# Kernel tuning notes

Hardware: AMD Instinct MI355X
Metric: run time of the kernel (lower is better)

Reference implementation:

```python
import jax, jax.numpy as jnp
import numpy as np

NUM_GROUPS = 32
EPS = 1e-5


def group_norm(x, gamma, beta):
    b, c, h, w = x.shape
    xg = x.reshape(b, NUM_GROUPS, c // NUM_GROUPS, h, w)
    mu = xg.mean(axis=(2, 3, 4), keepdims=True)
    var = xg.var(axis=(2, 3, 4), keepdims=True)
    xg = (xg - mu) * jax.lax.rsqrt(var + EPS)
    x = xg.reshape(b, c, h, w)
    return x * gamma[None, :, None, None] + beta[None, :, None, None]


def conv1x1(x, w, b):
    # 1x1 conv == per-pixel matmul over channels
    return jnp.einsum('oc,bchw->bohw', w, x) + b[None, :, None, None]


def setup_inputs() -> dict:
    key = jax.random.key(0)
    ks = jax.random.split(key, 6)
    c = 512
    scale = 0.02  # keep logits in a sane range
    return {
        'x': jax.random.normal(ks[0], (2, c, 64, 64), dtype=jnp.float32),
        'gn_w': jnp.ones((c,), jnp.float32),
        'gn_b': jnp.zeros((c,), jnp.float32),
        'wq': jax.random.normal(ks[1], (c, c), jnp.float32) * scale,
        'bq': jnp.zeros((c,), jnp.float32),
        'wk': jax.random.normal(ks[2], (c, c), jnp.float32) * scale,
        'bk': jnp.zeros((c,), jnp.float32),
        'wv': jax.random.normal(ks[3], (c, c), jnp.float32) * scale,
        'bv': jnp.zeros((c,), jnp.float32),
        'wo': jax.random.normal(ks[4], (c, c), jnp.float32) * scale,
        'bo': jnp.zeros((c,), jnp.float32),
    }


def reference(x, gn_w, gn_b, wq, bq, wk, bk, wv, bv, wo, bo):
    b, c, h, w = x.shape
    n = h * w
    h_ = group_norm(x, gn_w, gn_b)
    q = conv1x1(h_, wq, bq).reshape(b, c, n)  # (b,c,n)
    k = conv1x1(h_, wk, bk).reshape(b, c, n)
    v = conv1x1(h_, wv, bv).reshape(b, c, n)
    # scores: (b, n_q, n_k) = q^T k, scaled by c^-0.5
    scores = jnp.einsum('bcq,bck->bqk', q, k) * (c ** -0.5)
    attn = jax.nn.softmax(scores, axis=-1)
    # h_ = v @ attn^T  -> (b, c, n_q)
    out = jnp.einsum('bck,bqk->bcq', v, attn).reshape(b, c, h, w)
    return x + conv1x1(out, wo, bo)
```

## Files before the change

### kernel.cpp

```cpp
#include <hip/hip_runtime.h>

typedef __bf16 bf16_t;
typedef __bf16 bf16x8 __attribute__((ext_vector_type(8)));
typedef __bf16 bf16x4 __attribute__((ext_vector_type(4)));
typedef float  floatx4 __attribute__((ext_vector_type(4)));
typedef int    intx8  __attribute__((ext_vector_type(8)));

#define B_  2
#define C_  512
#define N_  4096
#define EPS 1e-5f
#define SCALE 0.044194173824159216f

__device__ __forceinline__ void gl2lds16(const void* g, void* l) {
  __builtin_amdgcn_global_load_lds(
      (const __attribute__((address_space(1))) void*)g,
      (__attribute__((address_space(3))) void*)l, 16, 0, 0);
}

__device__ __forceinline__ unsigned char f8(float x) {
  return (unsigned char)(__builtin_amdgcn_cvt_pk_fp8_f32(x, x, 0, false) & 0xff);
}

__device__ __forceinline__ floatx4 mfma128_fp8(intx8 a, intx8 b, floatx4 c) {
  return __builtin_amdgcn_mfma_scale_f32_16x16x128_f8f6f4(
      a, b, c, 0, 0, 0, 127, 0, 127);
}

union Frag32 { uint4 q[2]; intx8 v; };

template <int BM, int BN>
__device__ __forceinline__ void gemm_main(
    const bf16_t* __restrict__ A, const bf16_t* __restrict__ B, int K,
    int m0, int n0, floatx4 (&acc)[BM / 32][BN / 32],
    bf16_t* __restrict__ As, bf16_t* __restrict__ Bs) {
  const int tid = threadIdx.x;
  const int w = tid >> 6, l = tid & 63;
  const int wm = (w >> 1) * (BM / 2), wn = (w & 1) * (BN / 2);
  const int lrow = l & 15, lq = l >> 4;
  const int key = lrow & 7;
  const int slot0 = lq ^ key;
  const int slot1 = (4 + lq) ^ key;

  floatx4 zero = {0.f, 0.f, 0.f, 0.f};
#pragma unroll
  for (int mm = 0; mm < BM / 32; mm++)
#pragma unroll
    for (int nn = 0; nn < BN / 32; nn++) acc[mm][nn] = zero;

  for (int k0 = 0; k0 < K; k0 += 64) {
#pragma unroll
    for (int p = 0; p < BM / 32; p++) {
      int gch = p * 256 + tid;
      int r = gch >> 3;
      int cg = (gch & 7) ^ (r & 7);
      gl2lds16(A + (size_t)(m0 + r) * K + k0 + cg * 8, As + gch * 8);
    }
#pragma unroll
    for (int p = 0; p < BN / 32; p++) {
      int gch = p * 256 + tid;
      int r = gch >> 3;
      int cg = (gch & 7) ^ (r & 7);
      gl2lds16(B + (size_t)(n0 + r) * K + k0 + cg * 8, Bs + gch * 8);
    }
    __syncthreads();

    bf16x8 af[BM / 32][2], bfr[BN / 32][2];
#pragma unroll
    for (int mm = 0; mm < BM / 32; mm++) {
      int row = wm + mm * 16 + lrow;
      af[mm][0] = *(const bf16x8*)(As + row * 64 + slot0 * 8);
      af[mm][1] = *(const bf16x8*)(As + row * 64 + slot1 * 8);
    }
#pragma unroll
    for (int nn = 0; nn < BN / 32; nn++) {
      int row = wn + nn * 16 + lrow;
      bfr[nn][0] = *(const bf16x8*)(Bs + row * 64 + slot0 * 8);
      bfr[nn][1] = *(const bf16x8*)(Bs + row * 64 + slot1 * 8);
    }
#pragma unroll
    for (int h = 0; h < 2; h++)
#pragma unroll
      for (int mm = 0; mm < BM / 32; mm++)
#pragma unroll
        for (int nn = 0; nn < BN / 32; nn++)
          acc[mm][nn] = __builtin_amdgcn_mfma_f32_16x16x32_bf16(
              af[mm][h], bfr[nn][h], acc[mm][nn], 0, 0, 0);
    __syncthreads();
  }
}

__global__ __launch_bounds__(256) void gemm_qkv(
    const bf16_t* __restrict__ Wqkv, const bf16_t* __restrict__ h_t,
    unsigned char* __restrict__ q8, unsigned char* __restrict__ k8,
    unsigned char* __restrict__ v8,
    const float* __restrict__ bq, const float* __restrict__ bk,
    const float* __restrict__ bv) {
  __shared__ __align__(16) char smem[32768];
  floatx4 acc[4][4];
  const int m0 = blockIdx.y * 128, n0 = blockIdx.x * 128;
  gemm_main<128, 128>(Wqkv, h_t, 512, m0, n0, acc,
                      (bf16_t*)smem, (bf16_t*)(smem + 16384));

  const int tid = threadIdx.x, w = tid >> 6, l = tid & 63;
  const int wm = (w >> 1) * 64, wn = (w & 1) * 64;
  const int lrow = l & 15, q4 = (l >> 4) * 4;
  const int mat = m0 >> 9;
  const float* bias = (mat == 0) ? bq : (mat == 1) ? bk : bv;

  if (mat < 2) {
    unsigned char* ot = (mat == 0) ? q8 : k8;
#pragma unroll
    for (int mm = 0; mm < 4; mm++) {
#pragma unroll
      for (int nn = 0; nn < 4; nn++) {
        int n = n0 + wn + nn * 16 + lrow;
        int mloc = m0 - mat * 512 + wm + mm * 16 + q4;
        floatx4 a = acc[mm][nn];
        float v0 = a[0] + bias[mloc + 0];
        float v1 = a[1] + bias[mloc + 1];
        float v2 = a[2] + bias[mloc + 2];
        float v3 = a[3] + bias[mloc + 3];
        unsigned int p = __builtin_amdgcn_cvt_pk_fp8_f32(v0, v1, 0, false);
        p = __builtin_amdgcn_cvt_pk_fp8_f32(v2, v3, p, true);
        *(unsigned int*)(ot + (size_t)n * 512 + mloc) = p;
      }
    }
  } else {
    unsigned char* tile8 = (unsigned char*)smem;
#pragma unroll
    for (int mm = 0; mm < 4; mm++) {
#pragma unroll
      for (int nn = 0; nn < 4; nn++) {
        int colp = wn + nn * 16 + lrow;
        floatx4 a = acc[mm][nn];
#pragma unroll
        for (int r = 0; r < 4; r++) {
          int row = wm + mm * 16 + q4 + r;
          int ch = (colp >> 4) ^ ((row >> 2) & 7);
          tile8[row * 128 + ch * 16 + (colp & 15)] =
              f8(a[r] + bias[m0 - 1024 + row]);
        }
      }
    }
    __syncthreads();
    const int bb = n0 >> 12, nl0 = n0 & 4095;
    const int mloc0 = m0 - 1024;
#pragma unroll
    for (int i = 0; i < 4; i++) {
      int c = i * 256 + tid;
      int row = c >> 3, k = c & 7;
      int ch = k ^ ((row >> 2) & 7);
      uint4 d = *(const uint4*)(tile8 + row * 128 + ch * 16);
      *(uint4*)(v8 + (size_t)bb * (C_ * N_) + (size_t)(mloc0 + row) * N_ +
                nl0 + k * 16) = d;
    }
  }
}

__global__ __launch_bounds__(256) void gemm_scores(
    const unsigned char* __restrict__ q8, const unsigned char* __restrict__ k8,
    unsigned char* __restrict__ S8, size_t sstride, float* __restrict__ L,
    int zbase, int nz) {
  __shared__ __align__(16) unsigned char As[128 * 128];
  __shared__ __align__(16) unsigned char Bs[128 * 128];
  const int id = blockIdx.x;
  const int x = id & 7, s = id >> 3;
  const int mi = s & 3, n = (s >> 2) & 31;
  const int zloc = (nz == 2) ? (s >> 7) : 0;
  const int z = (nz == 2) ? zloc : zbase;
  const int m = x * 4 + mi;
  const int m0 = m * 128, n0 = n * 128;

  const unsigned char* A = k8 + (size_t)z * (N_ * C_);
  const unsigned char* B = q8 + (size_t)z * (N_ * C_);
  unsigned char* Sb = S8 + (size_t)zloc * sstride;
  float* Lb = L + (size_t)zloc * N_;

  const int tid = threadIdx.x;
  const int w = tid >> 6, l = tid & 63;
  const int wm = (w >> 1) * 64, wn = (w & 1) * 64;
  const int lrow = l & 15, lq = l >> 4;
  const int key = lrow & 7;
  const int e0 = (2 * lq) ^ key;

  floatx4 acc[4][4];
  floatx4 zero = {0.f, 0.f, 0.f, 0.f};
#pragma unroll
  for (int mm = 0; mm < 4; mm++)
#pragma unroll
    for (int nn = 0; nn < 4; nn++) acc[mm][nn] = zero;

  for (int k0 = 0; k0 < C_; k0 += 128) {
#pragma unroll
    for (int p = 0; p < 4; p++) {
      int gch = p * 256 + tid;
      int r = gch >> 3;
      int cg = (gch & 7) ^ (r & 7);
      gl2lds16(A + (size_t)(m0 + r) * C_ + k0 + cg * 16, As + gch * 16);
    }
#pragma unroll
    for (int p = 0; p < 4; p++) {
      int gch = p * 256 + tid;
      int r = gch >> 3;
      int cg = (gch & 7) ^ (r & 7);
      gl2lds16(B + (size_t)(n0 + r) * C_ + k0 + cg * 16, Bs + gch * 16);
    }
    __syncthreads();

    intx8 af[4], bfr[4];
#pragma unroll
    for (int mm = 0; mm < 4; mm++) {
      int row = wm + mm * 16 + lrow;
      Frag32 f;
      f.q[0] = *(const uint4*)(As + row * 128 + e0 * 16);
      f.q[1] = *(const uint4*)(As + row * 128 + (e0 ^ 1) * 16);
      af[mm] = f.v;
    }
#pragma unroll
    for (int nn = 0; nn < 4; nn++) {
      int row = wn + nn * 16 + lrow;
      Frag32 f;
      f.q[0] = *(const uint4*)(Bs + row * 128 + e0 * 16);
      f.q[1] = *(const uint4*)(Bs + row * 128 + (e0 ^ 1) * 16);
      bfr[nn] = f.v;
    }
#pragma unroll
    for (int mm = 0; mm < 4; mm++)
#pragma unroll
      for (int nn = 0; nn < 4; nn++)
        acc[mm][nn] = mfma128_fp8(af[mm], bfr[nn], acc[mm][nn]);
    __syncthreads();
  }

  float lsum[4] = {0.f, 0.f, 0.f, 0.f};
#pragma unroll
  for (int mm = 0; mm < 4; mm++) {
#pragma unroll
    for (int nn = 0; nn < 4; nn++) {
      int i  = n0 + wn + nn * 16 + lrow;
      int jb = m0 + wm + mm * 16 + lq * 4;
      floatx4 a = acc[mm][nn];
      float e0v = __expf(a[0] * SCALE);
      float e1v = __expf(a[1] * SCALE);
      float e2v = __expf(a[2] * SCALE);
      float e3v = __expf(a[3] * SCALE);
      lsum[nn] += (e0v + e1v) + (e2v + e3v);
      unsigned int p = __builtin_amdgcn_cvt_pk_fp8_f32(e0v, e1v, 0, false);
      p = __builtin_amdgcn_cvt_pk_fp8_f32(e2v, e3v, p, true);
      *(unsigned int*)(Sb + (size_t)i * N_ + jb) = p;
    }
  }
#pragma unroll
  for (int nn = 0; nn < 4; nn++) {
    float vsum = lsum[nn];
    vsum += __shfl_xor(vsum, 16);
    vsum += __shfl_xor(vsum, 32);
    if (lq == 0)
      atomicAdd(Lb + n0 + wn + nn * 16 + lrow, vsum);
  }
}

__global__ __launch_bounds__(512) void gemm_pv(
    const unsigned char* __restrict__ S8, size_t sstride,
    const unsigned char* __restrict__ v8, const float* __restrict__ L,
    bf16_t* __restrict__ O_t, int zbase, int nz) {
  __shared__ __align__(16) char smem[49152];
  const int id = blockIdx.x;
  int nb, mb, zloc;
  if (nz == 2) { nb = id >> 6; int g = id & 63; mb = g >> 1; zloc = g & 1; }
  else         { nb = id >> 5; mb = id & 31; zloc = 0; }
  const int z = (nz == 2) ? zloc : zbase;

  const unsigned char* A = S8 + (size_t)zloc * sstride;
  const unsigned char* B = v8 + (size_t)z * (C_ * N_);
  const float* Lb = L + (size_t)zloc * N_;
  const int m0 = mb * 128, n0 = nb * 64;

  const int tid = threadIdx.x;
  const int w = tid >> 6, l = tid & 63;
  const int wk = w >> 2;
  const int wl = w & 3;
  const int t2 = tid & 255;
  unsigned char* Ah = (unsigned char*)smem + wk * (128 * 128);
  unsigned char* Bh = (unsigned char*)(smem + 32768) + wk * (64 * 128);

  const int wm = (wl >> 1) * 64, wn = (wl & 1) * 32;
  const int lrow = l & 15, lq = l >> 4;
  const int key = lrow & 7;
  const int e0 = (2 * lq) ^ key;

  floatx4 acc[4][2];
  floatx4 zero = {0.f, 0.f, 0.f, 0.f};
#pragma unroll
  for (int mm = 0; mm < 4; mm++)
#pragma unroll
    for (int nn = 0; nn < 2; nn++) acc[mm][nn] = zero;

  const int kbase = wk * 2048;
  for (int kk = 0; kk < 2048; kk += 128) {
    const int k0 = kbase + kk;
#pragma unroll
    for (int p = 0; p < 4; p++) {
      int gch = p * 256 + t2;
      int r = gch >> 3;
      int cg = (gch & 7) ^ (r & 7);
      gl2lds16(A + (size_t)(m0 + r) * 4096 + k0 + cg * 16, Ah + gch * 16);
    }
#pragma unroll
    for (int p = 0; p < 2; p++) {
      int gch = p * 256 + t2;
      int r = gch >> 3;
      int cg = (gch & 7) ^ (r & 7);
      gl2lds16(B + (size_t)(n0 + r) * 4096 + k0 + cg * 16, Bh + gch * 16);
    }
    __syncthreads();

    intx8 af[4], bfr[2];
#pragma unroll
    for (int mm = 0; mm < 4; mm++) {
      int row = wm + mm * 16 + lrow;
      Frag32 f;
      f.q[0] = *(const uint4*)(Ah + row * 128 + e0 * 16);
      f.q[1] = *(const uint4*)(Ah + row * 128 + (e0 ^ 1) * 16);
      af[mm] = f.v;
    }
#pragma unroll
    for (int nn = 0; nn < 2; nn++) {
      int row = wn + nn * 16 + lrow;
      Frag32 f;
      f.q[0] = *(const uint4*)(Bh + row * 128 + e0 * 16);
      f.q[1] = *(const uint4*)(Bh + row * 128 + (e0 ^ 1) * 16);
      bfr[nn] = f.v;
    }
#pragma unroll
    for (int mm = 0; mm < 4; mm++)
#pragma unroll
      for (int nn = 0; nn < 2; nn++)
        acc[mm][nn] = mfma128_fp8(af[mm], bfr[nn], acc[mm][nn]);
    __syncthreads();
  }

  floatx4* buf = (floatx4*)smem;
  const int lanebase = wl * 64 + l;
  if (wk == 1) {
#pragma unroll
    for (int mm = 0; mm < 4; mm++)
#pragma unroll
      for (int nn = 0; nn < 2; nn++)
        buf[(mm * 2 + nn) * 256 + lanebase] = acc[mm][nn];
  }
  __syncthreads();

  bf16_t* tile = (bf16_t*)(smem + 32768);
  if (wk == 0) {
    const int q4 = lq * 4;
#pragma unroll
    for (int mm = 0; mm < 4; mm++) {
      const int rowb = wm + mm * 16 + q4;
      float rv0 = 1.0f / Lb[m0 + rowb + 0];
      float rv1 = 1.0f / Lb[m0 + rowb + 1];
      float rv2 = 1.0f / Lb[m0 + rowb + 2];
      float rv3 = 1.0f / Lb[m0 + rowb + 3];
#pragma unroll
      for (int nn = 0; nn < 2; nn++) {
        floatx4 a = acc[mm][nn] + buf[(mm * 2 + nn) * 256 + lanebase];
        a[0] *= rv0; a[1] *= rv1; a[2] *= rv2; a[3] *= rv3;
        int colp = wn + nn * 16 + lrow;
#pragma unroll
        for (int r = 0; r < 4; r++) {
          int row = rowb + r;
          int ch = (colp >> 3) ^ ((row >> 2) & 7);
          tile[row * 64 + ch * 8 + (colp & 7)] = (bf16_t)a[r];
        }
      }
    }
  }
  __syncthreads();
#pragma unroll
  for (int i = 0; i < 2; i++) {
    int c = i * 512 + tid;
    int row = c >> 3, k = c & 7;
    int ch = k ^ ((row >> 2) & 7);
    bf16x8 d = *(const bf16x8*)(tile + row * 64 + ch * 8);
    *(bf16x8*)(O_t + ((size_t)z * N_ + m0 + row) * C_ + n0 + k * 8) = d;
  }
}

__global__ __launch_bounds__(256) void gemm_final(
    const bf16_t* __restrict__ wo, const bf16_t* __restrict__ O_t,
    const float* __restrict__ bo, const float* __restrict__ x,
    float* __restrict__ out) {
  __shared__ __align__(16) char smem[32768];
  floatx4 acc[2][4];
  const int m0 = blockIdx.y * 64, n0 = blockIdx.x * 128;
  gemm_main<64, 128>(wo, O_t, 512, m0, n0, acc,
                     (bf16_t*)smem, (bf16_t*)(smem + 8192));

  const int tid = threadIdx.x, w = tid >> 6, l = tid & 63;
  const int wm = (w >> 1) * 32, wn = (w & 1) * 64;
  const int lrow = l & 15, q4 = (l >> 4) * 4;

  float* tile = (float*)smem;
#pragma unroll
  for (int mm = 0; mm < 2; mm++) {
#pragma unroll
    for (int nn = 0; nn < 4; nn++) {
      int colp = wn + nn * 16 + lrow;
      floatx4 a = acc[mm][nn];
#pragma unroll
      for (int r = 0; r < 4; r++) {
        int row = wm + mm * 16 + q4 + r;
        int ch = (colp >> 2) ^ ((row >> 2) & 31);
        tile[row * 128 + ch * 4 + (colp & 3)] = a[r] + bo[m0 + row];
      }
    }
  }
  __syncthreads();
  const int bb = n0 >> 12, nl0 = n0 & 4095;
#pragma unroll
  for (int i = 0; i < 8; i++) {
    int c = i * 256 + tid;
    int row = c >> 5, k = c & 31;
    int ch = k ^ ((row >> 2) & 31);
    float4 dv = *(const float4*)(tile + row * 128 + ch * 4);
    size_t off = ((size_t)(bb * C_ + m0 + row)) * N_ + nl0 + k * 4;
    float4 xv = *(const float4*)(x + off);
    dv.x += xv.x; dv.y += xv.y; dv.z += xv.z; dv.w += xv.w;
    *(float4*)(out + off) = dv;
  }
}

__global__ __launch_bounds__(256) void prep_kernel(
    const float* __restrict__ s0, const float* __restrict__ s1,
    const float* __restrict__ s2, const float* __restrict__ s3,
    bf16_t* __restrict__ d_qkv, bf16_t* __restrict__ d_o,
    const float* __restrict__ x, float2* __restrict__ part,
    float* __restrict__ L) {
  const int id = blockIdx.x;
  const int tid = threadIdx.x;
  __shared__ float rs[4], rss[4];
  if (id < 4096) {
    int i = id * 256 + tid;
    int mat = i >> 18, idx = i & 262143;
    const float* s = (mat == 0) ? s0 : (mat == 1) ? s1 : (mat == 2) ? s2 : s3;
    if (mat < 3)
      d_qkv[mat * 262144 + idx] = (bf16_t)s[idx];
    else
      d_o[idx] = (bf16_t)s[idx];
  } else if (id < 4608) {
    const int sid = id - 4096;
    const float4* xp = (const float4*)(x + (size_t)sid * 8192);
    float s = 0.f, ss = 0.f;
#pragma unroll
    for (int i = 0; i < 8; i++) {
      float4 v = xp[tid + i * 256];
      s += v.x + v.y + v.z + v.w;
      ss += v.x * v.x + v.y * v.y + v.z * v.z + v.w * v.w;
    }
#pragma unroll
    for (int off = 32; off; off >>= 1) {
      s += __shfl_down(s, off);
      ss += __shfl_down(ss, off);
    }
    if ((tid & 63) == 0) { rs[tid >> 6] = s; rss[tid >> 6] = ss; }
    __syncthreads();
    if (tid == 0) {
      float2 p;
      p.x = rs[0] + rs[1] + rs[2] + rs[3];
      p.y = rss[0] + rss[1] + rss[2] + rss[3];
      part[sid] = p;
    }
  } else {
    float4 z4 = {0.f, 0.f, 0.f, 0.f};
    float4* Lp = (float4*)L;
#pragma unroll
    for (int i = 0; i < 8; i++) Lp[tid + i * 256] = z4;
  }
}

__global__ __launch_bounds__(256) void zeroL_kernel(float* __restrict__ L) {
  float4 z4 = {0.f, 0.f, 0.f, 0.f};
  ((float4*)L)[blockIdx.x * 256 + threadIdx.x] = z4;
}

__global__ __launch_bounds__(256) void gn_apply(
    const float* __restrict__ x, const float* __restrict__ gamma,
    const float* __restrict__ beta, const float2* __restrict__ part,
    bf16_t* __restrict__ h_t) {
  const int id = blockIdx.x;
  const int nc = id & 15, g = (id >> 4) & 31, b = id >> 9;
  const int bg = b * 32 + g;
  float s = 0.f, ss = 0.f;
#pragma unroll
  for (int i = 0; i < 8; i++) {
    float2 p = part[bg * 8 + i];
    s += p.x; ss += p.y;
  }
  const float mean = s * (1.f / 65536.f);
  const float inv = rsqrtf(ss * (1.f / 65536.f) - mean * mean + EPS);

  __shared__ bf16_t tile[256 * 17];
  const int tid = threadIdx.x;
  const int n0 = nc * 256;
#pragma unroll
  for (int i = 0; i < 4; i++) {
    int lin = i * 256 + tid;
    int cl = lin >> 6;
    int n4 = (lin & 63) * 4;
    int c = g * 16 + cl;
    float ga = gamma[c], be = beta[c];
    float4 v = *(const float4*)(x + ((size_t)(b * C_ + c)) * N_ + n0 + n4);
    tile[(n4 + 0) * 17 + cl] = (bf16_t)((v.x - mean) * inv * ga + be);
    tile[(n4 + 1) * 17 + cl] = (bf16_t)((v.y - mean) * inv * ga + be);
    tile[(n4 + 2) * 17 + cl] = (bf16_t)((v.z - mean) * inv * ga + be);
    tile[(n4 + 3) * 17 + cl] = (bf16_t)((v.w - mean) * inv * ga + be);
  }
  __syncthreads();
  union { bf16_t h[8]; uint4 u; } p0, p1;
#pragma unroll
  for (int c = 0; c < 8; c++)  p0.h[c] = tile[tid * 17 + c];
#pragma unroll
  for (int c = 0; c < 8; c++)  p1.h[c] = tile[tid * 17 + 8 + c];
  bf16_t* dst = h_t + ((size_t)(b * N_ + n0 + tid)) * C_ + g * 16;
  *(uint4*)dst = p0.u;
  *(uint4*)(dst + 8) = p1.u;
}

extern "C" void kernel_launch(void* const* d_in, const int* in_sizes, int n_in,
                              void* d_out, int out_size, void* d_ws, size_t ws_size,
                              hipStream_t stream) {
  const float* x    = (const float*)d_in[0];
  const float* gn_w = (const float*)d_in[1];
  const float* gn_b = (const float*)d_in[2];
  const float* wq   = (const float*)d_in[3];
  const float* bq   = (const float*)d_in[4];
  const float* wk   = (const float*)d_in[5];
  const float* bk   = (const float*)d_in[6];
  const float* wv   = (const float*)d_in[7];
  const float* bv   = (const float*)d_in[8];
  const float* wo   = (const float*)d_in[9];
  const float* bo   = (const float*)d_in[10];
  float* out = (float*)d_out;

  char* ws = (char*)d_ws;
  bf16_t* h_t  = (bf16_t*)(ws);
  unsigned char* q8 = (unsigned char*)(ws + (8u << 20));
  unsigned char* k8 = (unsigned char*)(ws + (16u << 20));
  unsigned char* v8 = (unsigned char*)(ws + (24u << 20));
  bf16_t* O_t  = (bf16_t*)(ws + (32u << 20));
  bf16_t* wqkv = (bf16_t*)(ws + (40u << 20));
  bf16_t* wob  = (bf16_t*)(ws + (42u << 20));
  float2* gnp  = (float2*)(ws + (43u << 20));
  float*  L    = (float*)(ws + (43u << 20) + 8192);
  unsigned char* S8 = (unsigned char*)(ws + (44u << 20));

  const size_t SN = (size_t)N_ * N_;
  const int nz = (ws_size >= (44u << 20) + 2 * SN) ? 2 : 1;

  prep_kernel<<<4609, 256, 0, stream>>>(wq, wk, wv, wo, wqkv, wob, x, gnp, L);
  gn_apply<<<1024, 256, 0, stream>>>(x, gn_w, gn_b, gnp, h_t);

  gemm_qkv<<<dim3(64, 12), 256, 0, stream>>>(wqkv, h_t, q8, k8, v8,
                                             bq, bk, bv);

  if (nz == 2) {
    gemm_scores<<<2048, 256, 0, stream>>>(q8, k8, S8, SN, L, 0, 2);
    gemm_pv<<<512, 512, 0, stream>>>(S8, SN, v8, L, O_t, 0, 2);
  } else {
    for (int b = 0; b < B_; b++) {
      zeroL_kernel<<<4, 256, 0, stream>>>(L);
      gemm_scores<<<1024, 256, 0, stream>>>(q8, k8, S8, 0, L, b, 1);
      gemm_pv<<<256, 512, 0, stream>>>(S8, 0, v8, L, O_t, b, 1);
    }
  }

  gemm_final<<<dim3(64, 8), 256, 0, stream>>>(wob, O_t, bo, x, out);
}
```

Measured before the change: 189.4 us.

## Switch QKV and output projections to FP8 MFMA with scaled weights

Weights are quantized to FP8 with a 32x prescale, and the GroupNorm output and attention output are written as FP8 instead of bf16. The QKV and final projection GEMMs now use the scaled 16x16x128 FP8 MFMA with an exponent scale to undo the prescale, and the workspace layout is shrunk to match. This halves operand bytes and raises MFMA throughput for these GEMMs, at the cost of extra FP8 rounding error on activations and weights.

New measurement: 181.9 us. 1.04x faster.

```diff
diff --git a/kernel.cpp b/kernel.cpp
--- a/kernel.cpp
+++ b/kernel.cpp
@@ -2,7 +2,6 @@
 
 typedef __bf16 bf16_t;
 typedef __bf16 bf16x8 __attribute__((ext_vector_type(8)));
-typedef __bf16 bf16x4 __attribute__((ext_vector_type(4)));
 typedef float  floatx4 __attribute__((ext_vector_type(4)));
 typedef int    intx8  __attribute__((ext_vector_type(8)));
 
@@ -11,6 +10,8 @@
 #define N_  4096
 #define EPS 1e-5f
 #define SCALE 0.044194173824159216f
+#define SA_W 122
+#define SA_1 127
 
 __device__ __forceinline__ void gl2lds16(const void* g, void* l) {
   __builtin_amdgcn_global_load_lds(
@@ -21,90 +22,87 @@
 __device__ __forceinline__ unsigned char f8(float x) {
   return (unsigned char)(__builtin_amdgcn_cvt_pk_fp8_f32(x, x, 0, false) & 0xff);
 }
-
+__device__ __forceinline__ unsigned int pk4(float a, float b, float c, float d) {
+  unsigned int p = __builtin_amdgcn_cvt_pk_fp8_f32(a, b, 0, false);
+  return __builtin_amdgcn_cvt_pk_fp8_f32(c, d, p, true);
+}
+
+template <int SA, int SB>
 __device__ __forceinline__ floatx4 mfma128_fp8(intx8 a, intx8 b, floatx4 c) {
   return __builtin_amdgcn_mfma_scale_f32_16x16x128_f8f6f4(
-      a, b, c, 0, 0, 0, 127, 0, 127);
+      a, b, c, 0, 0, 0, SA, 0, SB);
 }
 
 union Frag32 { uint4 q[2]; intx8 v; };
 
-template <int BM, int BN>
-__device__ __forceinline__ void gemm_main(
-    const bf16_t* __restrict__ A, const bf16_t* __restrict__ B, int K,
-    int m0, int n0, floatx4 (&acc)[BM / 32][BN / 32],
-    bf16_t* __restrict__ As, bf16_t* __restrict__ Bs) {
-  const int tid = threadIdx.x;
-  const int w = tid >> 6, l = tid & 63;
-  const int wm = (w >> 1) * (BM / 2), wn = (w & 1) * (BN / 2);
-  const int lrow = l & 15, lq = l >> 4;
-  const int key = lrow & 7;
-  const int slot0 = lq ^ key;
-  const int slot1 = (4 + lq) ^ key;
-
-  floatx4 zero = {0.f, 0.f, 0.f, 0.f};
-#pragma unroll
-  for (int mm = 0; mm < BM / 32; mm++)
-#pragma unroll
-    for (int nn = 0; nn < BN / 32; nn++) acc[mm][nn] = zero;
-
-  for (int k0 = 0; k0 < K; k0 += 64) {
-#pragma unroll
-    for (int p = 0; p < BM / 32; p++) {
-      int gch = p * 256 + tid;
-      int r = gch >> 3;
-      int cg = (gch & 7) ^ (r & 7);
-      gl2lds16(A + (size_t)(m0 + r) * K + k0 + cg * 8, As + gch * 8);
-    }
-#pragma unroll
-    for (int p = 0; p < BN / 32; p++) {
-      int gch = p * 256 + tid;
-      int r = gch >> 3;
-      int cg = (gch & 7) ^ (r & 7);
-      gl2lds16(B + (size_t)(n0 + r) * K + k0 + cg * 8, Bs + gch * 8);
-    }
-    __syncthreads();
-
-    bf16x8 af[BM / 32][2], bfr[BN / 32][2];
-#pragma unroll
-    for (int mm = 0; mm < BM / 32; mm++) {
-      int row = wm + mm * 16 + lrow;
-      af[mm][0] = *(const bf16x8*)(As + row * 64 + slot0 * 8);
-      af[mm][1] = *(const bf16x8*)(As + row * 64 + slot1 * 8);
-    }
-#pragma unroll
-    for (int nn = 0; nn < BN / 32; nn++) {
-      int row = wn + nn * 16 + lrow;
-      bfr[nn][0] = *(const bf16x8*)(Bs + row * 64 + slot0 * 8);
-      bfr[nn][1] = *(const bf16x8*)(Bs + row * 64 + slot1 * 8);
-    }
-#pragma unroll
-    for (int h = 0; h < 2; h++)
-#pragma unroll
-      for (int mm = 0; mm < BM / 32; mm++)
-#pragma unroll
-        for (int nn = 0; nn < BN / 32; nn++)
-          acc[mm][nn] = __builtin_amdgcn_mfma_f32_16x16x32_bf16(
-              af[mm][h], bfr[nn][h], acc[mm][nn], 0, 0, 0);
-    __syncthreads();
-  }
-}
-
 __global__ __launch_bounds__(256) void gemm_qkv(
-    const bf16_t* __restrict__ Wqkv, const bf16_t* __restrict__ h_t,
+    const unsigned char* __restrict__ Wqkv8, const unsigned char* __restrict__ h8,
     unsigned char* __restrict__ q8, unsigned char* __restrict__ k8,
     unsigned char* __restrict__ v8,
     const float* __restrict__ bq, const float* __restrict__ bk,
     const float* __restrict__ bv) {
-  __shared__ __align__(16) char smem[32768];
+  __shared__ __align__(16) unsigned char smem[32768];
+  unsigned char* As = smem;
+  unsigned char* Bs = smem + 16384;
+  const int m0 = blockIdx.y * 128, n0 = blockIdx.x * 128;
+
+  const int tid = threadIdx.x;
+  const int w = tid >> 6, l = tid & 63;
+  const int wm = (w >> 1) * 64, wn = (w & 1) * 64;
+  const int lrow = l & 15, lq = l >> 4;
+  const int key = lrow & 7;
+  const int e0 = (2 * lq) ^ key;
+
   floatx4 acc[4][4];
-  const int m0 = blockIdx.y * 128, n0 = blockIdx.x * 128;
-  gemm_main<128, 128>(Wqkv, h_t, 512, m0, n0, acc,
-                      (bf16_t*)smem, (bf16_t*)(smem + 16384));
-
-  const int tid = threadIdx.x, w = tid >> 6, l = tid & 63;
-  const int wm = (w >> 1) * 64, wn = (w & 1) * 64;
-  const int lrow = l & 15, q4 = (l >> 4) * 4;
+  floatx4 zero = {0.f, 0.f, 0.f, 0.f};
+#pragma unroll
+  for (int mm = 0; mm < 4; mm++)
+#pragma unroll
+    for (int nn = 0; nn < 4; nn++) acc[mm][nn] = zero;
+
+  for (int k0 = 0; k0 < C_; k0 += 128) {
+#pragma unroll
+    for (int p = 0; p < 4; p++) {
+      int gch = p * 256 + tid;
+      int r = gch >> 3;
+      int cg = (gch & 7) ^ (r & 7);
+      gl2lds16(Wqkv8 + (size_t)(m0 + r) * C_ + k0 + cg * 16, As + gch * 16);
+    }
+#pragma unroll
+    for (int p = 0; p < 4; p++) {
+      int gch = p * 256 + tid;
+      int r = gch >> 3;
+      int cg = (gch & 7) ^ (r & 7);
+      gl2lds16(h8 + (size_t)(n0 + r) * C_ + k0 + cg * 16, Bs + gch * 16);
+    }
+    __syncthreads();
+
+    intx8 af[4], bfr[4];
+#pragma unroll
+    for (int mm = 0; mm < 4; mm++) {
+      int row = wm + mm * 16 + lrow;
+      Frag32 f;
+      f.q[0] = *(const uint4*)(As + row * 128 + e0 * 16);
+      f.q[1] = *(const uint4*)(As + row * 128 + (e0 ^ 1) * 16);
+      af[mm] = f.v;
+    }
+#pragma unroll
+    for (int nn = 0; nn < 4; nn++) {
+      int row = wn + nn * 16 + lrow;
+      Frag32 f;
+      f.q[0] = *(const uint4*)(Bs + row * 128 + e0 * 16);
+      f.q[1] = *(const uint4*)(Bs + row * 128 + (e0 ^ 1) * 16);
+      bfr[nn] = f.v;
+    }
+#pragma unroll
+    for (int mm = 0; mm < 4; mm++)
+#pragma unroll
+      for (int nn = 0; nn < 4; nn++)
+        acc[mm][nn] = mfma128_fp8<SA_W, SA_1>(af[mm], bfr[nn], acc[mm][nn]);
+    __syncthreads();
+  }
+
+  const int q4 = lq * 4;
   const int mat = m0 >> 9;
   const float* bias = (mat == 0) ? bq : (mat == 1) ? bk : bv;
 
@@ -117,17 +115,13 @@
         int n = n0 + wn + nn * 16 + lrow;
         int mloc = m0 - mat * 512 + wm + mm * 16 + q4;
         floatx4 a = acc[mm][nn];
-        float v0 = a[0] + bias[mloc + 0];
-        float v1 = a[1] + bias[mloc + 1];
-        float v2 = a[2] + bias[mloc + 2];
-        float v3 = a[3] + bias[mloc + 3];
-        unsigned int p = __builtin_amdgcn_cvt_pk_fp8_f32(v0, v1, 0, false);
-        p = __builtin_amdgcn_cvt_pk_fp8_f32(v2, v3, p, true);
+        unsigned int p = pk4(a[0] + bias[mloc + 0], a[1] + bias[mloc + 1],
+                             a[2] + bias[mloc + 2], a[3] + bias[mloc + 3]);
         *(unsigned int*)(ot + (size_t)n * 512 + mloc) = p;
       }
     }
   } else {
-    unsigned char* tile8 = (unsigned char*)smem;
+    unsigned char* tile8 = smem;
 #pragma unroll
     for (int mm = 0; mm < 4; mm++) {
 #pragma unroll
@@ -229,7 +223,7 @@
     for (int mm = 0; mm < 4; mm++)
 #pragma unroll
       for (int nn = 0; nn < 4; nn++)
-        acc[mm][nn] = mfma128_fp8(af[mm], bfr[nn], acc[mm][nn]);
+        acc[mm][nn] = mfma128_fp8<SA_1, SA_1>(af[mm], bfr[nn], acc[mm][nn]);
     __syncthreads();
   }
 
@@ -246,9 +240,7 @@
       float e2v = __expf(a[2] * SCALE);
       float e3v = __expf(a[3] * SCALE);
       lsum[nn] += (e0v + e1v) + (e2v + e3v);
-      unsigned int p = __builtin_amdgcn_cvt_pk_fp8_f32(e0v, e1v, 0, false);
-      p = __builtin_amdgcn_cvt_pk_fp8_f32(e2v, e3v, p, true);
-      *(unsigned int*)(Sb + (size_t)i * N_ + jb) = p;
+      *(unsigned int*)(Sb + (size_t)i * N_ + jb) = pk4(e0v, e1v, e2v, e3v);
     }
   }
 #pragma unroll
@@ -264,7 +256,7 @@
 __global__ __launch_bounds__(512) void gemm_pv(
     const unsigned char* __restrict__ S8, size_t sstride,
     const unsigned char* __restrict__ v8, const float* __restrict__ L,
-    bf16_t* __restrict__ O_t, int zbase, int nz) {
+    unsigned char* __restrict__ O8, int zbase, int nz) {
   __shared__ __align__(16) char smem[49152];
   const int id = blockIdx.x;
   int nb, mb, zloc;
@@ -337,7 +329,7 @@
     for (int mm = 0; mm < 4; mm++)
 #pragma unroll
       for (int nn = 0; nn < 2; nn++)
-        acc[mm][nn] = mfma128_fp8(af[mm], bfr[nn], acc[mm][nn]);
+        acc[mm][nn] = mfma128_fp8<SA_1, SA_1>(af[mm], bfr[nn], acc[mm][nn]);
     __syncthreads();
   }
 
@@ -383,24 +375,79 @@
     int row = c >> 3, k = c & 7;
     int ch = k ^ ((row >> 2) & 7);
     bf16x8 d = *(const bf16x8*)(tile + row * 64 + ch * 8);
-    *(bf16x8*)(O_t + ((size_t)z * N_ + m0 + row) * C_ + n0 + k * 8) = d;
+    uint2 p;
+    p.x = pk4((float)d[0], (float)d[1], (float)d[2], (float)d[3]);
+    p.y = pk4((float)d[4], (float)d[5], (float)d[6], (float)d[7]);
+    *(uint2*)(O8 + ((size_t)z * N_ + m0 + row) * C_ + n0 + k * 8) = p;
   }
 }
 
 __global__ __launch_bounds__(256) void gemm_final(
-    const bf16_t* __restrict__ wo, const bf16_t* __restrict__ O_t,
+    const unsigned char* __restrict__ wo8, const unsigned char* __restrict__ O8,
     const float* __restrict__ bo, const float* __restrict__ x,
     float* __restrict__ out) {
-  __shared__ __align__(16) char smem[32768];
+  __shared__ __align__(16) unsigned char smem[32768];
+  unsigned char* As = smem;
+  unsigned char* Bs = smem + 8192;
+  const int m0 = blockIdx.y * 64, n0 = blockIdx.x * 128;
+
+  const int tid = threadIdx.x;
+  const int w = tid >> 6, l = tid & 63;
+  const int wm = (w >> 1) * 32, wn = (w & 1) * 64;
+  const int lrow = l & 15, lq = l >> 4;
+  const int key = lrow & 7;
+  const int e0 = (2 * lq) ^ key;
+
   floatx4 acc[2][4];
-  const int m0 = blockIdx.y * 64, n0 = blockIdx.x * 128;
-  gemm_main<64, 128>(wo, O_t, 512, m0, n0, acc,
-                     (bf16_t*)smem, (bf16_t*)(smem + 8192));
-
-  const int tid = threadIdx.x, w = tid >> 6, l = tid & 63;
-  const int wm = (w >> 1) * 32, wn = (w & 1) * 64;
-  const int lrow = l & 15, q4 = (l >> 4) * 4;
-
+  floatx4 zero = {0.f, 0.f, 0.f, 0.f};
+#pragma unroll
+  for (int mm = 0; mm < 2; mm++)
+#pragma unroll
+    for (int nn = 0; nn < 4; nn++) acc[mm][nn] = zero;
+
+  for (int k0 = 0; k0 < C_; k0 += 128) {
+#pragma unroll
+    for (int p = 0; p < 2; p++) {
+      int gch = p * 256 + tid;
+      int r = gch >> 3;
+      int cg = (gch & 7) ^ (r & 7);
+      gl2lds16(wo8 + (size_t)(m0 + r) * C_ + k0 + cg * 16, As + gch * 16);
+    }
+#pragma unroll
+    for (int p = 0; p < 4; p++) {
+      int gch = p * 256 + tid;
+      int r = gch >> 3;
+      int cg = (gch & 7) ^ (r & 7);
+      gl2lds16(O8 + (size_t)(n0 + r) * C_ + k0 + cg * 16, Bs + gch * 16);
+    }
+    __syncthreads();
+
+    intx8 af[2], bfr[4];
+#pragma unroll
+    for (int mm = 0; mm < 2; mm++) {
+      int row = wm + mm * 16 + lrow;
+      Frag32 f;
+      f.q[0] = *(const uint4*)(As + row * 128 + e0 * 16);
+      f.q[1] = *(const uint4*)(As + row * 128 + (e0 ^ 1) * 16);
+      af[mm] = f.v;
+    }
+#pragma unroll
+    for (int nn = 0; nn < 4; nn++) {
+      int row = wn + nn * 16 + lrow;
+      Frag32 f;
+      f.q[0] = *(const uint4*)(Bs + row * 128 + e0 * 16);
+      f.q[1] = *(const uint4*)(Bs + row * 128 + (e0 ^ 1) * 16);
+      bfr[nn] = f.v;
+    }
+#pragma unroll
+    for (int mm = 0; mm < 2; mm++)
+#pragma unroll
+      for (int nn = 0; nn < 4; nn++)
+        acc[mm][nn] = mfma128_fp8<SA_W, SA_1>(af[mm], bfr[nn], acc[mm][nn]);
+    __syncthreads();
+  }
+
+  const int q4 = lq * 4;
   float* tile = (float*)smem;
 #pragma unroll
   for (int mm = 0; mm < 2; mm++) {
@@ -434,7 +481,7 @@
 __global__ __launch_bounds__(256) void prep_kernel(
     const float* __restrict__ s0, const float* __restrict__ s1,
     const float* __restrict__ s2, const float* __restrict__ s3,
-    bf16_t* __restrict__ d_qkv, bf16_t* __restrict__ d_o,
+    unsigned char* __restrict__ d_qkv8, unsigned char* __restrict__ d_o8,
     const float* __restrict__ x, float2* __restrict__ part,
     float* __restrict__ L) {
   const int id = blockIdx.x;
@@ -445,9 +492,9 @@
     int mat = i >> 18, idx = i & 262143;
     const float* s = (mat == 0) ? s0 : (mat == 1) ? s1 : (mat == 2) ? s2 : s3;
     if (mat < 3)
-      d_qkv[mat * 262144 + idx] = (bf16_t)s[idx];
+      d_qkv8[mat * 262144 + idx] = f8(s[idx] * 32.f);
     else
-      d_o[idx] = (bf16_t)s[idx];
+      d_o8[idx] = f8(s[idx] * 32.f);
   } else if (id < 4608) {
     const int sid = id - 4096;
     const float4* xp = (const float4*)(x + (size_t)sid * 8192);
@@ -487,7 +534,7 @@
 __global__ __launch_bounds__(256) void gn_apply(
     const float* __restrict__ x, const float* __restrict__ gamma,
     const float* __restrict__ beta, const float2* __restrict__ part,
-    bf16_t* __restrict__ h_t) {
+    unsigned char* __restrict__ h8) {
   const int id = blockIdx.x;
   const int nc = id & 15, g = (id >> 4) & 31, b = id >> 9;
   const int bg = b * 32 + g;
@@ -500,7 +547,7 @@
   const float mean = s * (1.f / 65536.f);
   const float inv = rsqrtf(ss * (1.f / 65536.f) - mean * mean + EPS);
 
-  __shared__ bf16_t tile[256 * 17];
+  __shared__ float tile[256 * 17];
   const int tid = threadIdx.x;
   const int n0 = nc * 256;
 #pragma unroll
@@ -511,20 +558,22 @@
     int c = g * 16 + cl;
     float ga = gamma[c], be = beta[c];
     float4 v = *(const float4*)(x + ((size_t)(b * C_ + c)) * N_ + n0 + n4);
-    tile[(n4 + 0) * 17 + cl] = (bf16_t)((v.x - mean) * inv * ga + be);
-    tile[(n4 + 1) * 17 + cl] = (bf16_t)((v.y - mean) * inv * ga + be);
-    tile[(n4 + 2) * 17 + cl] = (bf16_t)((v.z - mean) * inv * ga + be);
-    tile[(n4 + 3) * 17 + cl] = (bf16_t)((v.w - mean) * inv * ga + be);
+    tile[(n4 + 0) * 17 + cl] = (v.x - mean) * inv * ga + be;
+    tile[(n4 + 1) * 17 + cl] = (v.y - mean) * inv * ga + be;
+    tile[(n4 + 2) * 17 + cl] = (v.z - mean) * inv * ga + be;
+    tile[(n4 + 3) * 17 + cl] = (v.w - mean) * inv * ga + be;
   }
   __syncthreads();
-  union { bf16_t h[8]; uint4 u; } p0, p1;
-#pragma unroll
-  for (int c = 0; c < 8; c++)  p0.h[c] = tile[tid * 17 + c];
-#pragma unroll
-  for (int c = 0; c < 8; c++)  p1.h[c] = tile[tid * 17 + 8 + c];
-  bf16_t* dst = h_t + ((size_t)(b * N_ + n0 + tid)) * C_ + g * 16;
-  *(uint4*)dst = p0.u;
-  *(uint4*)(dst + 8) = p1.u;
+  uint4 p;
+  p.x = pk4(tile[tid * 17 + 0], tile[tid * 17 + 1],
+            tile[tid * 17 + 2], tile[tid * 17 + 3]);
+  p.y = pk4(tile[tid * 17 + 4], tile[tid * 17 + 5],
+            tile[tid * 17 + 6], tile[tid * 17 + 7]);
+  p.z = pk4(tile[tid * 17 + 8], tile[tid * 17 + 9],
+            tile[tid * 17 + 10], tile[tid * 17 + 11]);
+  p.w = pk4(tile[tid * 17 + 12], tile[tid * 17 + 13],
+            tile[tid * 17 + 14], tile[tid * 17 + 15]);
+  *(uint4*)(h8 + ((size_t)(b * N_ + n0 + tid)) * C_ + g * 16) = p;
 }
 
 extern "C" void kernel_launch(void* const* d_in, const int* in_sizes, int n_in,
@@ -544,36 +593,36 @@
   float* out = (float*)d_out;
 
   char* ws = (char*)d_ws;
-  bf16_t* h_t  = (bf16_t*)(ws);
-  unsigned char* q8 = (unsigned char*)(ws + (8u << 20));
-  unsigned char* k8 = (unsigned char*)(ws + (16u << 20));
-  unsigned char* v8 = (unsigned char*)(ws + (24u << 20));
-  bf16_t* O_t  = (bf16_t*)(ws + (32u << 20));
-  bf16_t* wqkv = (bf16_t*)(ws + (40u << 20));
-  bf16_t* wob  = (bf16_t*)(ws + (42u << 20));
-  float2* gnp  = (float2*)(ws + (43u << 20));
-  float*  L    = (float*)(ws + (43u << 20) + 8192);
-  unsigned char* S8 = (unsigned char*)(ws + (44u << 20));
+  unsigned char* h8    = (unsigned char*)(ws);
+  unsigned char* q8    = (unsigned char*)(ws + (4u << 20));
+  unsigned char* k8    = (unsigned char*)(ws + (8u << 20));
+  unsigned char* v8    = (unsigned char*)(ws + (12u << 20));
+  unsigned char* O8    = (unsigned char*)(ws + (16u << 20));
+  unsigned char* wqkv8 = (unsigned char*)(ws + (20u << 20));
+  unsigned char* wo8   = (unsigned char*)(ws + (21u << 20));
+  float2* gnp = (float2*)(ws + (22u << 20));
+  float*  L   = (float*)(ws + (22u << 20) + 8192);
+  unsigned char* S8 = (unsigned char*)(ws + (24u << 20));
 
   const size_t SN = (size_t)N_ * N_;
-  const int nz = (ws_size >= (44u << 20) + 2 * SN) ? 2 : 1;
-
-  prep_kernel<<<4609, 256, 0, stream>>>(wq, wk, wv, wo, wqkv, wob, x, gnp, L);
-  gn_apply<<<1024, 256, 0, stream>>>(x, gn_w, gn_b, gnp, h_t);
-
-  gemm_qkv<<<dim3(64, 12), 256, 0, stream>>>(wqkv, h_t, q8, k8, v8,
+  const int nz = (ws_size >= (24u << 20) + 2 * SN) ? 2 : 1;
+
+  prep_kernel<<<4609, 256, 0, stream>>>(wq, wk, wv, wo, wqkv8, wo8, x, gnp, L);
+  gn_apply<<<1024, 256, 0, stream>>>(x, gn_w, gn_b, gnp, h8);
+
+  gemm_qkv<<<dim3(64, 12), 256, 0, stream>>>(wqkv8, h8, q8, k8, v8,
                                              bq, bk, bv);
 
   if (nz == 2) {
     gemm_scores<<<2048, 256, 0, stream>>>(q8, k8, S8, SN, L, 0, 2);
-    gemm_pv<<<512, 512, 0, stream>>>(S8, SN, v8, L, O_t, 0, 2);
+    gemm_pv<<<512, 512, 0, stream>>>(S8, SN, v8, L, O8, 0, 2);
   } else {
     for (int b = 0; b < B_; b++) {
       zeroL_kernel<<<4, 256, 0, stream>>>(L);
       gemm_scores<<<1024, 256, 0, stream>>>(q8, k8, S8, 0, L, b, 1);
-      gemm_pv<<<256, 512, 0, stream>>>(S8, 0, v8, L, O_t, b, 1);
-    }
-  }
-
-  gemm_final<<<dim3(64, 8), 256, 0, stream>>>(wob, O_t, bo, x, out);
-}
+      gemm_pv<<<256, 512, 0, stream>>>(S8, 0, v8, L, O8, b, 1);
+    }
+  }
+
+  gemm_final<<<dim3(64, 8), 256, 0, stream>>>(wo8, O8, bo, x, out);
+}
```
